# Kernel optimization log

Measured on AMD Instinct MI355X. Metric: run time of the kernel, lower is better.

The kernel has to match this reference:

```python
import jax, jax.numpy as jnp
import numpy as np

HIDDEN = 1024
HEADS = 16
HEAD_DIM = HIDDEN // HEADS


def setup_inputs() -> dict:
    key = jax.random.key(0)
    ks = jax.random.split(key, 11)
    B, S = 2, 2048
    s = 1.0 / np.sqrt(HIDDEN)
    return {
        "query": jax.random.normal(ks[0], (B, S, HIDDEN), jnp.float32),
        "key": jax.random.normal(ks[1], (B, S, HIDDEN), jnp.float32),
        "value": jax.random.normal(ks[2], (B, S, HIDDEN), jnp.float32),
        "Wq": jax.random.uniform(ks[3], (HIDDEN, HIDDEN), jnp.float32, -s, s),
        "bq": jax.random.uniform(ks[4], (HIDDEN,), jnp.float32, -s, s),
        "Wk": jax.random.uniform(ks[5], (HIDDEN, HIDDEN), jnp.float32, -s, s),
        "bk": jax.random.uniform(ks[6], (HIDDEN,), jnp.float32, -s, s),
        "Wv": jax.random.uniform(ks[7], (HIDDEN, HIDDEN), jnp.float32, -s, s),
        "bv": jax.random.uniform(ks[8], (HIDDEN,), jnp.float32, -s, s),
        "Wo": jax.random.uniform(ks[9], (HIDDEN, HIDDEN), jnp.float32, -s, s),
        "bo": jax.random.uniform(ks[10], (HIDDEN,), jnp.float32, -s, s),
    }


def reference(query, key, value, Wq, bq, Wk, bk, Wv, bv, Wo, bo):
    B, Sq, _ = query.shape
    Sk = key.shape[1]
    # projections (torch Linear: x @ W^T + b)
    Q = (query @ Wq.T + bq).reshape(B, Sq, HEADS, HEAD_DIM).transpose(0, 2, 1, 3)
    K = (key @ Wk.T + bk).reshape(B, Sk, HEADS, HEAD_DIM).transpose(0, 2, 1, 3)
    V = (value @ Wv.T + bv).reshape(B, Sk, HEADS, HEAD_DIM).transpose(0, 2, 1, 3)
    scale = jnp.sqrt(jnp.float32(HEAD_DIM))
    scores = jnp.einsum("bhqd,bhkd->bhqk", Q, K) / scale  # [B,H,Sq,Sk]
    # causal mask (is_causal=True, Sq>1)
    causal = jnp.tril(jnp.ones((Sq, Sk), dtype=bool))
    scores = jnp.where(causal[None, None], scores, -jnp.inf)
    attn = jax.nn.softmax(scores, axis=-1)
    out = jnp.einsum("bhqk,bhkd->bhqd", attn, V)
    out = out.transpose(0, 2, 1, 3).reshape(B, Sq, HIDDEN)
    return out @ Wo.T + bo
```

## Files before the change

### kernel.cpp

```cpp
#include <hip/hip_runtime.h>
#include <hip/hip_bf16.h>


typedef __attribute__((ext_vector_type(4))) float f32x4;
typedef __attribute__((ext_vector_type(8))) short bf16x8;
typedef unsigned short u16;

#define SEQ   2048
#define NH    16
#define HD    64
#define HID   1024
#define CEXP  0.1803368801f
#define MEG   1048576u

static __device__ __forceinline__ u16 f2bf(float f) {
  union { __hip_bfloat16 h; u16 u; } c;
  c.h = __float2bfloat16(f);
  return c.u;
}

static __device__ __forceinline__ int swz(int row, int col8) {
  return col8 ^ ((row & 7) << 3);
}

static __device__ __forceinline__ void gll16(const void* g, void* l) {
  __builtin_amdgcn_global_load_lds(
      (const __attribute__((address_space(1))) void*)g,
      (__attribute__((address_space(3))) void*)l, 16, 0, 0);
}

__global__ __launch_bounds__(256) void cvt_kernel(
    const float* __restrict__ Wq, const float* __restrict__ Wk,
    const float* __restrict__ Wv, const float* __restrict__ Wo,
    const float* __restrict__ q, const float* __restrict__ k,
    const float* __restrict__ v,
    u16* __restrict__ wsout, u16* __restrict__ dob) {
  const int y = blockIdx.y;
  const int c = y & 3;
  const float* src;
  u16* dst;
  if (y < 4) {
    src = (y == 0) ? Wq : (y == 1) ? Wk : (y == 2) ? Wv : Wo;
    dst = wsout + (size_t)y * MEG;
  } else if (y < 8) {
    src = q + (size_t)c * MEG;
    dst = wsout + 4u * MEG + (size_t)c * MEG;
  } else if (y < 12) {
    src = k + (size_t)c * MEG;
    dst = dob + (size_t)c * MEG;
  } else {
    src = v + (size_t)c * MEG;
    dst = dob + 4u * MEG + (size_t)c * MEG;
  }
  int i = (blockIdx.x * 256 + threadIdx.x) * 4;
  float4 f = *(const float4*)(src + i);
  ushort4 o;
  o.x = f2bf(f.x); o.y = f2bf(f.y); o.z = f2bf(f.z); o.w = f2bf(f.w);
  *(ushort4*)(dst + i) = o;
}

__global__ __launch_bounds__(256) void proj_kernel(
    const u16* __restrict__ Xq, const u16* __restrict__ Xk,
    const u16* __restrict__ Xv, const u16* __restrict__ Wc,
    const float* __restrict__ bq, const float* __restrict__ bk,
    const float* __restrict__ bvp,
    u16* __restrict__ Qo, u16* __restrict__ Ko, u16* __restrict__ Vto) {
  __shared__ u16 As[128 * 64];
  __shared__ u16 Bs[128 * 64];

  const int tid  = threadIdx.x;
  const int lane = tid & 63;
  const int wid  = tid >> 6;
  const int wm   = wid >> 1, wn = wid & 1;
  const int l15  = lane & 15;
  const int lhi  = lane >> 4;
  const int z    = blockIdx.z;
  const int bm   = blockIdx.x * 128;
  const int bn   = blockIdx.y * 128;

  const u16* X = (z == 0) ? Xq : (z == 1) ? Xk : Xv;
  const u16* W = Wc + (size_t)z * (HID * HID);
  const float* bias = (z == 0) ? bq : (z == 1) ? bk : bvp;

  f32x4 acc[4][4];
#pragma unroll
  for (int i = 0; i < 4; i++)
#pragma unroll
    for (int j = 0; j < 4; j++) acc[i][j] = (f32x4){0.f, 0.f, 0.f, 0.f};

  const int lrow  = lane >> 3;
  const int gcol8 = lane & 7;

  for (int t = 0; t < 16; t++) {
    const int k0 = t * 64;
#pragma unroll
    for (int c = 0; c < 4; c++) {
      const int row  = c * 32 + wid * 8 + lrow;
      const int scol = (gcol8 ^ (row & 7)) * 8;
      gll16(X + (size_t)(bm + row) * HID + k0 + scol,
            (char*)As + c * 4096 + wid * 1024);
      gll16(W + (size_t)(bn + row) * HID + k0 + scol,
            (char*)Bs + c * 4096 + wid * 1024);
    }
    __syncthreads();
#pragma unroll
    for (int ks = 0; ks < 2; ks++) {
      bf16x8 af[4], bfm[4];
#pragma unroll
      for (int i = 0; i < 4; i++) {
        const int row = wm * 64 + i * 16 + l15;
        af[i] = *(const bf16x8*)&As[row * 64 + swz(row, ks * 32 + lhi * 8)];
      }
#pragma unroll
      for (int j = 0; j < 4; j++) {
        const int row = wn * 64 + j * 16 + l15;
        bfm[j] = *(const bf16x8*)&Bs[row * 64 + swz(row, ks * 32 + lhi * 8)];
      }
#pragma unroll
      for (int i = 0; i < 4; i++)
#pragma unroll
        for (int j = 0; j < 4; j++)
          acc[i][j] = __builtin_amdgcn_mfma_f32_16x16x32_bf16(af[i], bfm[j], acc[i][j], 0, 0, 0);
    }
    __syncthreads();
  }

  const int bb = bm >> 11;
#pragma unroll
  for (int j = 0; j < 4; j++) {
    const int n = bn + wn * 64 + j * 16 + l15;
    const float bv_ = bias[n];
    const int h = n >> 6, d = n & 63;
    if (z == 2) {
#pragma unroll
      for (int i = 0; i < 4; i++) {
        const int s0 = (bm + wm * 64 + i * 16 + lhi * 4) & 2047;
        ushort4 t;
        t.x = f2bf(acc[i][j][0] + bv_);
        t.y = f2bf(acc[i][j][1] + bv_);
        t.z = f2bf(acc[i][j][2] + bv_);
        t.w = f2bf(acc[i][j][3] + bv_);
        *(ushort4*)&Vto[((size_t)(bb * NH + h) * HD + d) * SEQ + s0] = t;
      }
    } else {
      u16* O = z ? Ko : Qo;
#pragma unroll
      for (int i = 0; i < 4; i++)
#pragma unroll
        for (int r = 0; r < 4; r++) {
          const int m = bm + wm * 64 + i * 16 + lhi * 4 + r;
          const int s = m & 2047;
          O[(((size_t)(bb * NH + h) * SEQ + s) << 6) + d] = f2bf(acc[i][j][r] + bv_);
        }
    }
  }
}

__global__ __launch_bounds__(512) void attn_kernel(
    const u16* __restrict__ Q, const u16* __restrict__ K,
    const u16* __restrict__ Vt, u16* __restrict__ Aout) {
  __shared__ __align__(16) char pool[51200];

  const int tid  = threadIdx.x;
  const int lane = tid & 63;
  const int wid  = tid >> 6;
  const int rw   = wid & 3;
  const int g    = wid >> 2;
  const int l15  = lane & 15;
  const int lhi  = lane >> 4;

  const int flat = blockIdx.x;
  const int slot = flat >> 3;
  const int bh   = (flat & 7) * 4 + (slot & 3);
  const int qt   = 31 - (slot >> 2);
  const int b    = bh >> 4, h = bh & 15;
  const size_t base = (size_t)bh * SEQ * HD;

  u16* Ksh = (u16*)(pool + g * 8192);
  u16* Vsh = (u16*)(pool + 16384 + g * 8192);
  u16* Psh = (u16*)(pool + 32768 + wid * 2304);

  const int qrow = qt * 64 + rw * 16 + l15;
  bf16x8 aq[2];
  aq[0] = *(const bf16x8*)&Q[base + (size_t)qrow * HD + lhi * 8];
  aq[1] = *(const bf16x8*)&Q[base + (size_t)qrow * HD + 32 + lhi * 8];

  f32x4 o[4];
#pragma unroll
  for (int n = 0; n < 4; n++) o[n] = (f32x4){0.f, 0.f, 0.f, 0.f};
  float m_s = -1e30f, l_s = 0.f;

  const int gt   = tid & 255;
  const int srow = gt >> 2;
  const int sd   = (gt & 3) * 16;

  bf16x8 pk0, pk1, pv0, pv1;

#define ATTN_LOAD(kt_)                                                            \
  {                                                                               \
    const u16* kp = K + base + (size_t)((kt_) * 64 + srow) * HD + sd;             \
    pk0 = *(const bf16x8*)kp;                                                     \
    pk1 = *(const bf16x8*)(kp + 8);                                               \
    const u16* vp = Vt + base + (size_t)srow * SEQ + (kt_) * 64 + sd;             \
    pv0 = *(const bf16x8*)vp;                                                     \
    pv1 = *(const bf16x8*)(vp + 8);                                               \
  }

  if (g <= qt) ATTN_LOAD(g);

  const int nsteps = qt / 2 + 1;
  for (int it = 0; it < nsteps; ++it) {
    const int kt = 2 * it + g;
    const bool act = (kt <= qt);
    __syncthreads();
    if (act) {
      *(bf16x8*)&Ksh[srow * 64 + swz(srow, sd)]     = pk0;
      *(bf16x8*)&Ksh[srow * 64 + swz(srow, sd + 8)] = pk1;
      *(bf16x8*)&Vsh[srow * 64 + swz(srow, sd)]     = pv0;
      *(bf16x8*)&Vsh[srow * 64 + swz(srow, sd + 8)] = pv1;
    }
    const int ktn = kt + 2;
    if (ktn <= qt) ATTN_LOAD(ktn);
    __syncthreads();
    if (act) {
      f32x4 sc[4];
      __builtin_amdgcn_s_setprio(1);
#pragma unroll
      for (int n = 0; n < 4; n++) {
        sc[n] = (f32x4){0.f, 0.f, 0.f, 0.f};
#pragma unroll
        for (int ks = 0; ks < 2; ks++) {
          const int krow = n * 16 + l15;
          bf16x8 bk = *(const bf16x8*)&Ksh[krow * 64 + swz(krow, ks * 32 + lhi * 8)];
          sc[n] = __builtin_amdgcn_mfma_f32_16x16x32_bf16(bk, aq[ks], sc[n], 0, 0, 0);
        }
      }
      __builtin_amdgcn_s_setprio(0);
      if (kt == qt) {
#pragma unroll
        for (int n = 0; n < 4; n++)
#pragma unroll
          for (int r = 0; r < 4; r++)
            if (kt * 64 + n * 16 + lhi * 4 + r > qrow) sc[n][r] = -1e30f;
      }
      float mx = -1e30f;
#pragma unroll
      for (int n = 0; n < 4; n++)
        mx = fmaxf(mx, fmaxf(fmaxf(sc[n][0], sc[n][1]), fmaxf(sc[n][2], sc[n][3])));
      mx = fmaxf(mx, __shfl_xor(mx, 16, 64));
      mx = fmaxf(mx, __shfl_xor(mx, 32, 64));
      if (__any(mx > m_s + 64.0f)) {
        const float mnew = fmaxf(m_s, mx);
        const float fac = __builtin_amdgcn_exp2f((m_s - mnew) * CEXP);
        l_s *= fac;
        m_s = mnew;
        float facr[4];
#pragma unroll
        for (int r = 0; r < 4; r++) facr[r] = __shfl(fac, lhi * 4 + r, 64);
#pragma unroll
        for (int n = 0; n < 4; n++) {
          o[n][0] *= facr[0]; o[n][1] *= facr[1];
          o[n][2] *= facr[2]; o[n][3] *= facr[3];
        }
      }
      const float nmc = -m_s * CEXP;
      float ps = 0.f;
      u16 pb[4][4];
#pragma unroll
      for (int n = 0; n < 4; n++)
#pragma unroll
        for (int r = 0; r < 4; r++) {
          const float e = __builtin_amdgcn_exp2f(fmaf(sc[n][r], CEXP, nmc));
          ps += e;
          pb[n][r] = f2bf(e);
        }
      ps += __shfl_xor(ps, 16, 64);
      ps += __shfl_xor(ps, 32, 64);
      l_s += ps;
#pragma unroll
      for (int n = 0; n < 4; n++) {
        ushort4 t; t.x = pb[n][0]; t.y = pb[n][1]; t.z = pb[n][2]; t.w = pb[n][3];
        *(ushort4*)&Psh[l15 * 72 + n * 16 + lhi * 4] = t;
      }
      bf16x8 ap0 = *(const bf16x8*)&Psh[l15 * 72 + lhi * 8];
      bf16x8 ap1 = *(const bf16x8*)&Psh[l15 * 72 + 32 + lhi * 8];
      __builtin_amdgcn_s_setprio(1);
#pragma unroll
      for (int n = 0; n < 4; n++) {
        const int vrow = n * 16 + l15;
        bf16x8 bv0 = *(const bf16x8*)&Vsh[vrow * 64 + swz(vrow, lhi * 8)];
        bf16x8 bv1 = *(const bf16x8*)&Vsh[vrow * 64 + swz(vrow, 32 + lhi * 8)];
        o[n] = __builtin_amdgcn_mfma_f32_16x16x32_bf16(ap0, bv0, o[n], 0, 0, 0);
        o[n] = __builtin_amdgcn_mfma_f32_16x16x32_bf16(ap1, bv1, o[n], 0, 0, 0);
      }
      __builtin_amdgcn_s_setprio(0);
    }
  }
#undef ATTN_LOAD

  __syncthreads();
  float m_o[4], l_o[4];
#pragma unroll
  for (int r = 0; r < 4; r++) {
    m_o[r] = __shfl(m_s, lhi * 4 + r, 64);
    l_o[r] = __shfl(l_s, lhi * 4 + r, 64);
  }

  f32x4* comb = (f32x4*)pool;
  const int ci = (rw * 64 + lane) * 6;
  if (g == 0) {
#pragma unroll
    for (int n = 0; n < 4; n++) comb[ci + n] = o[n];
    comb[ci + 4] = (f32x4){m_o[0], m_o[1], m_o[2], m_o[3]};
    comb[ci + 5] = (f32x4){l_o[0], l_o[1], l_o[2], l_o[3]};
  }
  __syncthreads();
  if (g == 1) {
    f32x4 m0 = comb[ci + 4];
    f32x4 l0 = comb[ci + 5];
    float a0[4], a1[4], inv[4];
#pragma unroll
    for (int r = 0; r < 4; r++) {
      const float m = fmaxf(m0[r], m_o[r]);
      a0[r] = __builtin_amdgcn_exp2f((m0[r] - m) * CEXP);
      a1[r] = __builtin_amdgcn_exp2f((m_o[r] - m) * CEXP);
      inv[r] = 1.0f / (l0[r] * a0[r] + l_o[r] * a1[r]);
    }
#pragma unroll
    for (int n = 0; n < 4; n++) {
      f32x4 o0 = comb[ci + n];
#pragma unroll
      for (int r = 0; r < 4; r++) {
        const int rowg = qt * 64 + rw * 16 + lhi * 4 + r;
        const float val = (o0[r] * a0[r] + o[n][r] * a1[r]) * inv[r];
        Aout[(((size_t)(b * SEQ + rowg)) << 10) + h * 64 + n * 16 + l15] = f2bf(val);
      }
    }
  }
}

__global__ __launch_bounds__(256) void oproj_kernel(
    const u16* __restrict__ X, const u16* __restrict__ W,
    const float* __restrict__ bias, float* __restrict__ Out) {
  __shared__ u16 As[128 * 64];
  __shared__ u16 Bs[64 * 64];

  const int tid  = threadIdx.x;
  const int lane = tid & 63;
  const int wid  = tid >> 6;
  const int wm   = wid >> 1, wn = wid & 1;
  const int l15  = lane & 15;
  const int lhi  = lane >> 4;
  const int bm   = blockIdx.x * 128;
  const int bn   = blockIdx.y * 64;

  f32x4 acc[4][2];
#pragma unroll
  for (int i = 0; i < 4; i++)
#pragma unroll
    for (int j = 0; j < 2; j++) acc[i][j] = (f32x4){0.f, 0.f, 0.f, 0.f};

  const int lrow  = lane >> 3;
  const int gcol8 = lane & 7;

  for (int t = 0; t < 16; t++) {
    const int k0 = t * 64;
#pragma unroll
    for (int c = 0; c < 4; c++) {
      const int row  = c * 32 + wid * 8 + lrow;
      const int scol = (gcol8 ^ (row & 7)) * 8;
      gll16(X + (size_t)(bm + row) * HID + k0 + scol,
            (char*)As + c * 4096 + wid * 1024);
      if (c < 2)
        gll16(W + (size_t)(bn + row) * HID + k0 + scol,
              (char*)Bs + c * 4096 + wid * 1024);
    }
    __syncthreads();
#pragma unroll
    for (int ks = 0; ks < 2; ks++) {
      bf16x8 af[4], bfm[2];
#pragma unroll
      for (int i = 0; i < 4; i++) {
        const int row = wm * 64 + i * 16 + l15;
        af[i] = *(const bf16x8*)&As[row * 64 + swz(row, ks * 32 + lhi * 8)];
      }
#pragma unroll
      for (int j = 0; j < 2; j++) {
        const int row = wn * 32 + j * 16 + l15;
        bfm[j] = *(const bf16x8*)&Bs[row * 64 + swz(row, ks * 32 + lhi * 8)];
      }
#pragma unroll
      for (int i = 0; i < 4; i++)
#pragma unroll
        for (int j = 0; j < 2; j++)
          acc[i][j] = __builtin_amdgcn_mfma_f32_16x16x32_bf16(af[i], bfm[j], acc[i][j], 0, 0, 0);
    }
    __syncthreads();
  }

#pragma unroll
  for (int j = 0; j < 2; j++) {
    const int n = bn + wn * 32 + j * 16 + l15;
    const float bv_ = bias[n];
#pragma unroll
    for (int i = 0; i < 4; i++)
#pragma unroll
      for (int r = 0; r < 4; r++) {
        const int m = bm + wm * 64 + i * 16 + lhi * 4 + r;
        Out[(size_t)m * HID + n] = acc[i][j][r] + bv_;
      }
  }
}

extern "C" void kernel_launch(void* const* d_in, const int* in_sizes, int n_in,
                              void* d_out, int out_size, void* d_ws, size_t ws_size,
                              hipStream_t stream) {
  const float* q  = (const float*)d_in[0];
  const float* k  = (const float*)d_in[1];
  const float* v  = (const float*)d_in[2];
  const float* Wq = (const float*)d_in[3];
  const float* bq = (const float*)d_in[4];
  const float* Wk = (const float*)d_in[5];
  const float* bk = (const float*)d_in[6];
  const float* Wv = (const float*)d_in[7];
  const float* bv = (const float*)d_in[8];
  const float* Wo = (const float*)d_in[9];
  const float* bo = (const float*)d_in[10];

  u16* ws   = (u16*)d_ws;
  u16* wqkv = ws;
  u16* wob  = ws + 3u * MEG;
  u16* qb   = ws + 4u * MEG;
  u16* Qb   = ws + 8u * MEG;
  u16* Kb   = ws + 12u * MEG;
  u16* Vtb  = ws + 16u * MEG;
  u16* Ab   = qb;
  u16* kbf  = (u16*)d_out;
  u16* vbf  = (u16*)d_out + 4u * MEG;

  cvt_kernel<<<dim3(1024, 16), 256, 0, stream>>>(Wq, Wk, Wv, Wo, q, k, v, ws, kbf);

  proj_kernel<<<dim3(32, 8, 3), 256, 0, stream>>>(qb, kbf, vbf, wqkv, bq, bk, bv,
                                                  Qb, Kb, Vtb);

  attn_kernel<<<dim3(1024), 512, 0, stream>>>(Qb, Kb, Vtb, Ab);

  oproj_kernel<<<dim3(32, 16), 256, 0, stream>>>(Ab, wob, bo, (float*)d_out);
}
```

Before: 117.1 us.

## Fuse fp32-to-bf16 activation conversion into QKV projection loads, shrink N tile

Stops pre-converting q/k/v activations to bf16 in a separate pass. The projection kernel now loads fp32 activations directly, converts them in registers and writes them swizzled into LDS, while weights still use direct global-to-LDS loads. The N tile is halved to 64 to double the grid and offset the lower per-block work. This removes a full read/write pass over 48MB of activations, but each projection block now reads fp32 A (twice the bytes) and re-reads it across 16 N-blocks instead of 8.

Result: slower. 166.4 us (+42.1%).

```diff
diff --git a/kernel.cpp b/kernel.cpp
--- a/kernel.cpp
+++ b/kernel.cpp
@@ -32,41 +32,25 @@
 __global__ __launch_bounds__(256) void cvt_kernel(
     const float* __restrict__ Wq, const float* __restrict__ Wk,
     const float* __restrict__ Wv, const float* __restrict__ Wo,
-    const float* __restrict__ q, const float* __restrict__ k,
-    const float* __restrict__ v,
-    u16* __restrict__ wsout, u16* __restrict__ dob) {
+    u16* __restrict__ dst) {
   const int y = blockIdx.y;
-  const int c = y & 3;
-  const float* src;
-  u16* dst;
-  if (y < 4) {
-    src = (y == 0) ? Wq : (y == 1) ? Wk : (y == 2) ? Wv : Wo;
-    dst = wsout + (size_t)y * MEG;
-  } else if (y < 8) {
-    src = q + (size_t)c * MEG;
-    dst = wsout + 4u * MEG + (size_t)c * MEG;
-  } else if (y < 12) {
-    src = k + (size_t)c * MEG;
-    dst = dob + (size_t)c * MEG;
-  } else {
-    src = v + (size_t)c * MEG;
-    dst = dob + 4u * MEG + (size_t)c * MEG;
-  }
+  const float* src = (y == 0) ? Wq : (y == 1) ? Wk : (y == 2) ? Wv : Wo;
+  u16* d = dst + (size_t)y * MEG;
   int i = (blockIdx.x * 256 + threadIdx.x) * 4;
   float4 f = *(const float4*)(src + i);
   ushort4 o;
   o.x = f2bf(f.x); o.y = f2bf(f.y); o.z = f2bf(f.z); o.w = f2bf(f.w);
-  *(ushort4*)(dst + i) = o;
+  *(ushort4*)(d + i) = o;
 }
 
 __global__ __launch_bounds__(256) void proj_kernel(
-    const u16* __restrict__ Xq, const u16* __restrict__ Xk,
-    const u16* __restrict__ Xv, const u16* __restrict__ Wc,
+    const float* __restrict__ Xq, const float* __restrict__ Xk,
+    const float* __restrict__ Xv, const u16* __restrict__ Wc,
     const float* __restrict__ bq, const float* __restrict__ bk,
     const float* __restrict__ bvp,
     u16* __restrict__ Qo, u16* __restrict__ Ko, u16* __restrict__ Vto) {
   __shared__ u16 As[128 * 64];
-  __shared__ u16 Bs[128 * 64];
+  __shared__ u16 Bs[64 * 64];
 
   const int tid  = threadIdx.x;
   const int lane = tid & 63;
@@ -76,50 +60,64 @@
   const int lhi  = lane >> 4;
   const int z    = blockIdx.z;
   const int bm   = blockIdx.x * 128;
-  const int bn   = blockIdx.y * 128;
-
-  const u16* X = (z == 0) ? Xq : (z == 1) ? Xk : Xv;
+  const int bn   = blockIdx.y * 64;
+
+  const float* X = (z == 0) ? Xq : (z == 1) ? Xk : Xv;
   const u16* W = Wc + (size_t)z * (HID * HID);
   const float* bias = (z == 0) ? bq : (z == 1) ? bk : bvp;
 
-  f32x4 acc[4][4];
+  f32x4 acc[4][2];
 #pragma unroll
   for (int i = 0; i < 4; i++)
 #pragma unroll
-    for (int j = 0; j < 4; j++) acc[i][j] = (f32x4){0.f, 0.f, 0.f, 0.f};
-
+    for (int j = 0; j < 2; j++) acc[i][j] = (f32x4){0.f, 0.f, 0.f, 0.f};
+
+  const int arow  = tid >> 1;
+  const int acol0 = (tid & 1) * 32;
   const int lrow  = lane >> 3;
   const int gcol8 = lane & 7;
 
   for (int t = 0; t < 16; t++) {
     const int k0 = t * 64;
 #pragma unroll
-    for (int c = 0; c < 4; c++) {
+    for (int c = 0; c < 2; c++) {
       const int row  = c * 32 + wid * 8 + lrow;
       const int scol = (gcol8 ^ (row & 7)) * 8;
-      gll16(X + (size_t)(bm + row) * HID + k0 + scol,
-            (char*)As + c * 4096 + wid * 1024);
       gll16(W + (size_t)(bn + row) * HID + k0 + scol,
             (char*)Bs + c * 4096 + wid * 1024);
     }
+    {
+      const float* xp = X + (size_t)(bm + arow) * HID + k0 + acol0;
+#pragma unroll
+      for (int c = 0; c < 4; c++) {
+        float4 f0 = ((const float4*)xp)[c * 2 + 0];
+        float4 f1 = ((const float4*)xp)[c * 2 + 1];
+        ushort4 h0, h1;
+        h0.x = f2bf(f0.x); h0.y = f2bf(f0.y); h0.z = f2bf(f0.z); h0.w = f2bf(f0.w);
+        h1.x = f2bf(f1.x); h1.y = f2bf(f1.y); h1.z = f2bf(f1.z); h1.w = f2bf(f1.w);
+        u16* dst = &As[arow * 64 + swz(arow, acol0 + c * 8)];
+        *(ushort4*)(dst + 0) = h0;
+        *(ushort4*)(dst + 4) = h1;
+      }
+    }
     __syncthreads();
 #pragma unroll
     for (int ks = 0; ks < 2; ks++) {
-      bf16x8 af[4], bfm[4];
+      bf16x8 af[4], bfm[2];
 #pragma unroll
       for (int i = 0; i < 4; i++) {
         const int row = wm * 64 + i * 16 + l15;
         af[i] = *(const bf16x8*)&As[row * 64 + swz(row, ks * 32 + lhi * 8)];
       }
 #pragma unroll
-      for (int j = 0; j < 4; j++) {
-        const int row = wn * 64 + j * 16 + l15;
+      for (int j = 0; j < 2; j++) {
+        const int row = wn * 32 + j * 16 + l15;
         bfm[j] = *(const bf16x8*)&Bs[row * 64 + swz(row, ks * 32 + lhi * 8)];
       }
 #pragma unroll
       for (int i = 0; i < 4; i++)
 #pragma unroll
-        for (int j = 0; j < 4; j++)
+        for (int j = 0; j < 2; j++)
           acc[i][j] = __builtin_amdgcn_mfma_f32_16x16x32_bf16(af[i], bfm[j], acc[i][j], 0, 0, 0);
     }
     __syncthreads();
@@ -127,8 +125,8 @@
 
   const int bb = bm >> 11;
 #pragma unroll
-  for (int j = 0; j < 4; j++) {
-    const int n = bn + wn * 64 + j * 16 + l15;
+  for (int j = 0; j < 2; j++) {
+    const int n = bn + wn * 32 + j * 16 + l15;
     const float bv_ = bias[n];
     const int h = n >> 6, d = n & 63;
     if (z == 2) {
@@ -430,18 +428,15 @@
   u16* ws   = (u16*)d_ws;
   u16* wqkv = ws;
   u16* wob  = ws + 3u * MEG;
-  u16* qb   = ws + 4u * MEG;
-  u16* Qb   = ws + 8u * MEG;
-  u16* Kb   = ws + 12u * MEG;
-  u16* Vtb  = ws + 16u * MEG;
-  u16* Ab   = qb;
-  u16* kbf  = (u16*)d_out;
-  u16* vbf  = (u16*)d_out + 4u * MEG;
-
-  cvt_kernel<<<dim3(1024, 16), 256, 0, stream>>>(Wq, Wk, Wv, Wo, q, k, v, ws, kbf);
-
-  proj_kernel<<<dim3(32, 8, 3), 256, 0, stream>>>(qb, kbf, vbf, wqkv, bq, bk, bv,
-                                                  Qb, Kb, Vtb);
+  u16* Qb   = ws + 4u * MEG;
+  u16* Kb   = ws + 8u * MEG;
+  u16* Vtb  = ws + 12u * MEG;
+  u16* Ab   = ws + 16u * MEG;
+
+  cvt_kernel<<<dim3(1024, 4), 256, 0, stream>>>(Wq, Wk, Wv, Wo, ws);
+
+  proj_kernel<<<dim3(32, 16, 3), 256, 0, stream>>>(q, k, v, wqkv, bq, bk, bv,
+                                                   Qb, Kb, Vtb);
 
   attn_kernel<<<dim3(1024), 512, 0, stream>>>(Qb, Kb, Vtb, Ab);
 
```
